# Performance work log

Hardware: AMD Instinct MI355X
Metric: run time of the kernel (lower is better)

The kernel has to match this reference:

```python
import jax, jax.numpy as jnp
import numpy as np

B, C, D, W, H = 8, 256, 24, 24, 24
COUT = 256
EMBED = 128
HEADS = 8
WORD = 64
POOL = 3  # forward hardcodes adaptive_avg_pool3d(x, 3)


def setup_inputs() -> dict:
    key = jax.random.key(0)
    ks = jax.random.split(key, 12)
    s = lambda n: 1.0 / np.sqrt(n)
    return {
        "x": jax.random.normal(ks[0], (B, C, D, W, H), dtype=jnp.float32),
        "qk_w": jax.random.normal(ks[1], (2 * EMBED, POOL ** 3), dtype=jnp.float32) * s(POOL ** 3),
        "qk_b": jax.random.normal(ks[2], (2 * EMBED,), dtype=jnp.float32) * 0.02,
        "wq_w": jax.random.normal(ks[3], (HEADS * WORD, EMBED), dtype=jnp.float32) * s(EMBED),
        "wq_b": jax.random.normal(ks[4], (HEADS * WORD,), dtype=jnp.float32) * 0.02,
        "wk_w": jax.random.normal(ks[5], (HEADS * WORD, EMBED), dtype=jnp.float32) * s(EMBED),
        "wk_b": jax.random.normal(ks[6], (HEADS * WORD,), dtype=jnp.float32) * 0.02,
        "fch_w": jax.random.normal(ks[7], (1, HEADS), dtype=jnp.float32) * s(HEADS),
        "fch_b": jax.random.normal(ks[8], (1,), dtype=jnp.float32) * 0.02,
        "conv_w": jax.random.normal(ks[9], (COUT, C), dtype=jnp.float32) * s(C),
        "conv_b": jax.random.normal(ks[10], (COUT,), dtype=jnp.float32) * 0.02,
    }


def reference(x, qk_w, qk_b, wq_w, wq_b, wk_w, wk_b, fch_w, fch_b, conv_w, conv_b):
    b, c, d, w, h = x.shape
    # adaptive_avg_pool3d to 3x3x3 (exact: dims divisible by 3) -> [b, c, 27]
    xmean = x.reshape(b, c, POOL, d // POOL, POOL, w // POOL, POOL, h // POOL)
    xmean = xmean.mean(axis=(3, 5, 7)).reshape(b, c, POOL ** 3)
    # qk projection -> split into q, k of [b, c, embed]
    qk = xmean @ qk_w.T + qk_b                      # [b, c, 2*embed]
    qk = qk.reshape(b, c, 2, EMBED)
    q, k = qk[:, :, 0], qk[:, :, 1]
    # head projections -> [b, heads, c, word]
    q = (q @ wq_w.T + wq_b).reshape(b, c, HEADS, WORD).transpose(0, 2, 1, 3)
    k = (k @ wk_w.T + wk_b).reshape(b, c, HEADS, WORD).transpose(0, 2, 1, 3)
    # channel attention: scores over channels [b, heads, c, c]
    scores = jnp.einsum("bhcw,bhkw->bhck", q / jnp.sqrt(jnp.float32(WORD)), k)
    attn = jax.nn.softmax(scores, axis=-1)          # dropout is identity in eval
    # v is the raw spatial map [b, c, d*w*h]; broadcast over heads
    v = x.reshape(b, c, d * w * h)
    y = jnp.einsum("bhck,bkn->bhcn", attn, v)       # [b, heads, c, dwh]
    # fch: Linear(heads, 1) combining heads
    y = jnp.einsum("bhcn,h->bcn", y, fch_w[0]) + fch_b[0]
    y = y.reshape(b, c, d, w, h)
    attn_out = jnp.einsum("bhck,h->bck", attn, fch_w[0]) + fch_b[0]  # [b, c, c]
    # 1x1x1 conv residual
    out = jnp.einsum("bcxyz,oc->boxyz", y + x, conv_w) + conv_b[None, :, None, None, None]
    return (out, attn_out)
```

## Files before the change

### kernel.cpp

```cpp
#include <hip/hip_runtime.h>
#include <cstdint>
#include <cstddef>

#define B_    8
#define C_    256
#define DWH   13824
#define P3    27
#define COUT_ 256

#define OFF_XMEAN 0
#define OFF_WQT   55296
#define OFF_WKT   69120
#define OFF_BQ    82944
#define OFF_BK    83456
#define OFF_BETA  83968
#define OFF_G     84224
#define OFF_U     90272
#define OFF_V     90488
#define OFF_D     90704
#define OFF_ZT    90712
#define OFF_A     549464
#define OFF_MPH   1073752
#define OFF_MPL   1335896

typedef __attribute__((ext_vector_type(8))) short bf16x8;
typedef __attribute__((ext_vector_type(4))) float f32x4;

__device__ __forceinline__ void split_bf16(float v, unsigned short& h, unsigned short& l) {
    unsigned u  = __float_as_uint(v);
    unsigned hu = u & 0xFFFF0000u;
    float r = v - __uint_as_float(hu);
    h = (unsigned short)(u >> 16);
    l = (unsigned short)(__float_as_uint(r) >> 16);
}

__device__ __forceinline__ unsigned rne2(float a, float b) {
    unsigned ua = __float_as_uint(a), ub = __float_as_uint(b);
    unsigned ra = (ua + 0x7FFFu + ((ua >> 16) & 1u)) >> 16;
    unsigned rb = (ub + 0x7FFFu + ((ub >> 16) & 1u)) >> 16;
    return ra | (rb << 16);
}

__global__ __launch_bounds__(256) void k_pool(const float* __restrict__ x,
                                              float* __restrict__ xmean) {
    int bc = blockIdx.x;
    __shared__ float p0[576], p1[576], p2[576];
    __shared__ float part[216];
    const float* xb = x + (size_t)bc * DWH;
    for (int t = threadIdx.x; t < 576; t += 256) {
        int g  = t >> 6;
        int s  = t & 63;
        int pd = g / 3, pw = g % 3;
        int d  = pd * 8 + (s >> 3);
        int w  = pw * 8 + (s & 7);
        const float4* r = (const float4*)(xb + ((size_t)d * 24 + w) * 24);
        float4 f0 = r[0], f1 = r[1], f2 = r[2], f3 = r[3], f4v = r[4], f5 = r[5];
        p0[t] = f0.x + f0.y + f0.z + f0.w + f1.x + f1.y + f1.z + f1.w;
        p1[t] = f2.x + f2.y + f2.z + f2.w + f3.x + f3.y + f3.z + f3.w;
        p2[t] = f4v.x + f4v.y + f4v.z + f4v.w + f5.x + f5.y + f5.z + f5.w;
    }
    __syncthreads();
    int tid = threadIdx.x;
    if (tid < 216) {
        int cell = tid >> 3, seg = tid & 7;
        int pd = cell / 9, pw = (cell / 3) % 3, ph = cell % 3;
        int g = pd * 3 + pw;
        const float* src = (ph == 0) ? p0 : (ph == 1 ? p1 : p2);
        float s = 0.f;
        #pragma unroll
        for (int i = 0; i < 8; ++i) s += src[g * 64 + seg * 8 + i];
        part[tid] = s;
    }
    __syncthreads();
    if (tid < 27) {
        float s = 0.f;
        #pragma unroll
        for (int i = 0; i < 8; ++i) s += part[tid * 8 + i];
        xmean[(size_t)bc * P3 + tid] = s * (1.0f / 512.0f);
    }
}

__global__ __launch_bounds__(128) void k_combine(
    const float* __restrict__ qk_w, const float* __restrict__ qk_b,
    const float* __restrict__ wq_w, const float* __restrict__ wq_b,
    const float* __restrict__ wk_w, const float* __restrict__ wk_b,
    float* __restrict__ WqT, float* __restrict__ WkT,
    float* __restrict__ bq, float* __restrict__ bk) {
    int t = blockIdx.x * 128 + threadIdx.x;
    if (t < 13824) {
        int j = t / 27, p = t % 27;
        float s = 0.f;
        for (int e = 0; e < 128; ++e) s += wq_w[j * 128 + e] * qk_w[e * 27 + p];
        WqT[p * 512 + j] = s;
    } else if (t < 27648) {
        int u = t - 13824, j = u / 27, p = u % 27;
        float s = 0.f;
        for (int e = 0; e < 128; ++e) s += wk_w[j * 128 + e] * qk_w[(128 + e) * 27 + p];
        WkT[p * 512 + j] = s;
    } else if (t < 28160) {
        int j = t - 27648;
        float s = wq_b[j];
        for (int e = 0; e < 128; ++e) s += wq_w[j * 128 + e] * qk_b[e];
        bq[j] = s;
    } else if (t < 28672) {
        int j = t - 28160;
        float s = wk_b[j];
        for (int e = 0; e < 128; ++e) s += wk_w[j * 128 + e] * qk_b[128 + e];
        bk[j] = s;
    }
}

__global__ __launch_bounds__(256) void k_G(
    const float* __restrict__ WqT, const float* __restrict__ WkT,
    const float* __restrict__ bq, const float* __restrict__ bk,
    float* __restrict__ G, float* __restrict__ U,
    float* __restrict__ V, float* __restrict__ D) {
    int h = blockIdx.x;
    int idx = blockIdx.y * 256 + threadIdx.x;
    int base = h * 64;
    if (idx < 756) {
        int p = idx / 28, r = idx % 28;
        float s = 0.f;
        if (r < 27) {
            #pragma unroll 8
            for (int w = 0; w < 64; ++w)
                s += WqT[p * 512 + base + w] * WkT[r * 512 + base + w];
        }
        G[(h * 27 + p) * 28 + r] = 0.125f * s;
    } else if (idx < 783) {
        int p = idx - 756;
        float s = 0.f;
        #pragma unroll 8
        for (int w = 0; w < 64; ++w) s += WqT[p * 512 + base + w] * bk[base + w];
        V[h * 27 + p] = 0.125f * s;
    } else if (idx < 810) {
        int r = idx - 783;
        float s = 0.f;
        #pragma unroll 8
        for (int w = 0; w < 64; ++w) s += WkT[r * 512 + base + w] * bq[base + w];
        U[h * 27 + r] = 0.125f * s;
    } else if (idx == 810) {
        float s = 0.f;
        #pragma unroll 8
        for (int w = 0; w < 64; ++w) s += bq[base + w] * bk[base + w];
        D[h] = 0.125f * s;
    }
}

__global__ __launch_bounds__(256) void k_z(
    const float* __restrict__ xmean, const float* __restrict__ G,
    const float* __restrict__ U, const float* __restrict__ V,
    const float* __restrict__ D, float* __restrict__ ZT) {
    int h = blockIdx.x, b = blockIdx.y;
    int k = threadIdx.x;
    __shared__ float Gs[756], Us[27], Vs[27], Ds;
    for (int idx = threadIdx.x; idx < 756; idx += 256) Gs[idx] = G[h * 756 + idx];
    if (threadIdx.x < 27) { Us[threadIdx.x] = U[h * 27 + threadIdx.x];
                            Vs[threadIdx.x] = V[h * 27 + threadIdx.x]; }
    if (threadIdx.x == 27) Ds = D[h];
    __syncthreads();
    float xm[28];
    const float* xp = xmean + ((size_t)(b * C_) + k) * P3;
    #pragma unroll
    for (int r = 0; r < 27; ++r) xm[r] = xp[r];
    xm[27] = 0.f;
    float z[28];
    #pragma unroll
    for (int p = 0; p < 27; ++p) {
        float acc = Vs[p];
        #pragma unroll
        for (int r4 = 0; r4 < 7; ++r4) {
            float4 g = *(const float4*)&Gs[p * 28 + r4 * 4];
            acc += g.x * xm[r4 * 4] + g.y * xm[r4 * 4 + 1]
                 + g.z * xm[r4 * 4 + 2] + g.w * xm[r4 * 4 + 3];
        }
        z[p] = acc;
    }
    {
        float e = Ds;
        #pragma unroll
        for (int r = 0; r < 27; ++r) e += Us[r] * xm[r];
        z[27] = e;
    }
    float4* zt = (float4*)ZT;
    int bh = b * 8 + h;
    #pragma unroll
    for (int p4 = 0; p4 < 7; ++p4) {
        float4 v = {z[p4 * 4], z[p4 * 4 + 1], z[p4 * 4 + 2], z[p4 * 4 + 3]};
        zt[((size_t)(bh * 7 + p4)) * 256 + k] = v;
    }
}

__global__ __launch_bounds__(256) void k_attn(
    const float* __restrict__ xmean, const float* __restrict__ ZT,
    const float* __restrict__ fch_w, const float* __restrict__ fch_b,
    float* __restrict__ A, float* __restrict__ attn_out) {
    int b = blockIdx.y;
    int c0 = blockIdx.x * 4;
    int t = threadIdx.x;
    int lane = t & 63, wv = t >> 6;
    __shared__ float xsh[4 * 28];
    __shared__ float ss[4][256];
    __shared__ float mx[4], den[4];
    if (t < 112) {
        int i = t / 28, p = t % 28;
        xsh[t] = (p < 27) ? xmean[((size_t)(b * C_) + c0 + i) * P3 + p] : 1.0f;
    }
    __syncthreads();
    float4 xr[4][7];
    #pragma unroll
    for (int cl = 0; cl < 4; ++cl)
        #pragma unroll
        for (int p4 = 0; p4 < 7; ++p4)
            xr[cl][p4] = *(const float4*)&xsh[cl * 28 + p4 * 4];
    float areg[4] = {0.f, 0.f, 0.f, 0.f};
    const float4* zt = (const float4*)ZT;
    for (int h = 0; h < 8; ++h) {
        int bh = b * 8 + h;
        float4 zk[7];
        #pragma unroll
        for (int p4 = 0; p4 < 7; ++p4)
            zk[p4] = zt[((size_t)(bh * 7 + p4)) * 256 + t];
        #pragma unroll
        for (int cl = 0; cl < 4; ++cl) {
            float dot = 0.f;
            #pragma unroll
            for (int p4 = 0; p4 < 7; ++p4) {
                float4 xv = xr[cl][p4];
                float4 zv = zk[p4];
                dot += xv.x * zv.x + xv.y * zv.y + xv.z * zv.z + xv.w * zv.w;
            }
            ss[cl][t] = dot;
        }
        __syncthreads();
        {
            int cl = wv;
            float4 v = *(const float4*)&ss[cl][lane * 4];
            float m = fmaxf(fmaxf(v.x, v.y), fmaxf(v.z, v.w));
            for (int off = 32; off; off >>= 1) m = fmaxf(m, __shfl_xor(m, off, 64));
            float s = expf(v.x - m) + expf(v.y - m) + expf(v.z - m) + expf(v.w - m);
            for (int off = 32; off; off >>= 1) s += __shfl_xor(s, off, 64);
            if (lane == 0) { mx[cl] = m; den[cl] = s; }
        }
        __syncthreads();
        float fw = fch_w[h];
        #pragma unroll
        for (int cl = 0; cl < 4; ++cl)
            areg[cl] += expf(ss[cl][t] - mx[cl]) * (fw / den[cl]);
        __syncthreads();
    }
    float fb = fch_b[0];
    #pragma unroll
    for (int cl = 0; cl < 4; ++cl) {
        size_t idx = ((size_t)(b * C_) + c0 + cl) * C_ + t;
        A[idx] = areg[cl];
        attn_out[idx] = areg[cl] + fb;
    }
}

__global__ __launch_bounds__(256) void k_M(
    const float* __restrict__ A, const float* __restrict__ conv_w,
    const float* __restrict__ fch_b, const float* __restrict__ conv_b,
    unsigned short* __restrict__ MpH, unsigned short* __restrict__ MpL,
    float* __restrict__ beta) {
    int b = blockIdx.y;
    int o0 = blockIdx.x * 8;
    int t = threadIdx.x;
    __shared__ float cw[8][256];
    #pragma unroll
    for (int r = 0; r < 8; ++r) cw[r][t] = conv_w[(o0 + r) * 256 + t];
    __syncthreads();
    float acc[8] = {0.f, 0.f, 0.f, 0.f, 0.f, 0.f, 0.f, 0.f};
    const float* Ab = A + (size_t)b * C_ * C_;
    for (int c = 0; c < 256; ++c) {
        float av = Ab[(size_t)c * 256 + t];
        #pragma unroll
        for (int r = 0; r < 8; ++r) acc[r] += cw[r][c] * av;
    }
    if (b == 0 && t < 8) {
        float s = 0.f;
        for (int c = 0; c < 256; ++c) s += cw[t][c];
        beta[o0 + t] = fch_b[0] * s + conv_b[o0 + t];
    }
    int ks = t >> 5, e = t & 7;
    int lanehi = ((t >> 3) & 3) << 4;
    size_t base = ((size_t)(b * 8 + ks) * 16 + (o0 >> 4)) * 64;
    int osub = (o0 & 8);
    #pragma unroll
    for (int r = 0; r < 8; ++r) {
        float mv = acc[r] + cw[r][t];
        unsigned short h, l;
        split_bf16(mv, h, l);
        size_t idx = (base + ((osub + r) | lanehi)) * 8 + e;
        MpH[idx] = h;
        MpL[idx] = l;
    }
}

__global__ __launch_bounds__(256, 3) void k_out_mfma(
    const bf16x8* __restrict__ MpH, const bf16x8* __restrict__ MpL,
    const float* __restrict__ x, const float* __restrict__ beta,
    float* __restrict__ out) {
    int b  = blockIdx.y;
    int n0 = blockIdx.x * 64;
    int t  = threadIdx.x;
    int lane = t & 63, wv = t >> 6;
    int l15  = lane & 15;
    int kseg = lane >> 4;

    __shared__ __align__(16) unsigned short Xs[2][64 * 32];

    f32x4 acc[4][4];
    #pragma unroll
    for (int m = 0; m < 4; ++m)
        #pragma unroll
        for (int nf = 0; nf < 4; ++nf) acc[m][nf] = (f32x4){0.f, 0.f, 0.f, 0.f};

    const float* xb = x + (size_t)b * 256 * DWH;
    const bf16x8* mh = MpH + (size_t)b * 8192;
    const bf16x8* ml = MpL + (size_t)b * 8192;

    int sn = t & 63;
    int sk = t >> 6;
    const float* xcol0 = xb + (size_t)(sk * 8) * DWH + n0 + sn;
    int soff = sn * 64 + ((sk * 16) ^ (((sn >> 1) & 3) << 4));

    {
        float xr[8];
        #pragma unroll
        for (int j = 0; j < 8; ++j) xr[j] = xcol0[(size_t)j * DWH];
        uint4 v;
        v.x = rne2(xr[0], xr[1]); v.y = rne2(xr[2], xr[3]);
        v.z = rne2(xr[4], xr[5]); v.w = rne2(xr[6], xr[7]);
        *(uint4*)((char*)Xs[0] + soff) = v;
    }
    __syncthreads();

    for (int s = 0; s < 8; ++s) {
        int cur = s & 1;
        float xn[8];
        if (s < 7) {
            const float* xc = xcol0 + (size_t)((s + 1) * 32) * DWH;
            #pragma unroll
            for (int j = 0; j < 8; ++j) xn[j] = xc[(size_t)j * DWH];
        }
        bf16x8 Ah[4], Al[4];
        #pragma unroll
        for (int m = 0; m < 4; ++m) {
            int idx = (s * 16 + wv * 4 + m) * 64 + lane;
            Ah[m] = mh[idx];
            Al[m] = ml[idx];
        }
        bf16x8 Bf[4];
        #pragma unroll
        for (int nf = 0; nf < 4; ++nf) {
            int n = nf * 16 + l15;
            int off = n * 64 + ((kseg * 16) ^ (((n >> 1) & 3) << 4));
            Bf[nf] = *(const bf16x8*)((const char*)Xs[cur] + off);
        }
        #pragma unroll
        for (int m = 0; m < 4; ++m)
            #pragma unroll
            for (int nf = 0; nf < 4; ++nf) {
                f32x4 c = acc[m][nf];
                c = __builtin_amdgcn_mfma_f32_16x16x32_bf16(Bf[nf], Al[m], c, 0, 0, 0);
                c = __builtin_amdgcn_mfma_f32_16x16x32_bf16(Bf[nf], Ah[m], c, 0, 0, 0);
                acc[m][nf] = c;
            }
        if (s < 7) {
            uint4 v;
            v.x = rne2(xn[0], xn[1]); v.y = rne2(xn[2], xn[3]);
            v.z = rne2(xn[4], xn[5]); v.w = rne2(xn[6], xn[7]);
            *(uint4*)((char*)Xs[cur ^ 1] + soff) = v;
        }
        __syncthreads();
    }

    int r4 = (lane >> 4) * 4;
    int wo = wv * 64;
    #pragma unroll
    for (int m = 0; m < 4; ++m) {
        int o = wo + m * 16 + l15;
        float bet = beta[o];
        float* orow = out + ((size_t)(b * 256 + o)) * DWH + n0 + r4;
        #pragma unroll
        for (int nf = 0; nf < 4; ++nf) {
            f32x4 c = acc[m][nf];
            float4 v = {c[0] + bet, c[1] + bet, c[2] + bet, c[3] + bet};
            *(float4*)(orow + nf * 16) = v;
        }
    }
}

extern "C" void kernel_launch(void* const* d_in, const int* in_sizes, int n_in,
                              void* d_out, int out_size, void* d_ws, size_t ws_size,
                              hipStream_t stream) {
    const float* x      = (const float*)d_in[0];
    const float* qk_w   = (const float*)d_in[1];
    const float* qk_b   = (const float*)d_in[2];
    const float* wq_w   = (const float*)d_in[3];
    const float* wq_b   = (const float*)d_in[4];
    const float* wk_w   = (const float*)d_in[5];
    const float* wk_b   = (const float*)d_in[6];
    const float* fch_w  = (const float*)d_in[7];
    const float* fch_b  = (const float*)d_in[8];
    const float* conv_w = (const float*)d_in[9];
    const float* conv_b = (const float*)d_in[10];
    float* out = (float*)d_out;
    float* attn_out = out + (size_t)B_ * COUT_ * DWH;
    float* ws = (float*)d_ws;
    unsigned short* MpH = (unsigned short*)(ws + OFF_MPH);
    unsigned short* MpL = (unsigned short*)(ws + OFF_MPL);

    k_pool<<<B_ * C_, 256, 0, stream>>>(x, ws + OFF_XMEAN);
    k_combine<<<224, 128, 0, stream>>>(qk_w, qk_b, wq_w, wq_b, wk_w, wk_b,
                                       ws + OFF_WQT, ws + OFF_WKT,
                                       ws + OFF_BQ, ws + OFF_BK);
    k_G<<<dim3(8, 4), 256, 0, stream>>>(ws + OFF_WQT, ws + OFF_WKT,
                                        ws + OFF_BQ, ws + OFF_BK,
                                        ws + OFF_G, ws + OFF_U, ws + OFF_V, ws + OFF_D);
    k_z<<<dim3(8, B_), 256, 0, stream>>>(ws + OFF_XMEAN, ws + OFF_G, ws + OFF_U,
                                         ws + OFF_V, ws + OFF_D, ws + OFF_ZT);
    k_attn<<<dim3(64, B_), 256, 0, stream>>>(ws + OFF_XMEAN, ws + OFF_ZT, fch_w, fch_b,
                                             ws + OFF_A, attn_out);
    k_M<<<dim3(32, B_), 256, 0, stream>>>(ws + OFF_A, conv_w, fch_b, conv_b,
                                          MpH, MpL, ws + OFF_BETA);
    k_out_mfma<<<dim3(216, B_), 256, 0, stream>>>((const bf16x8*)MpH, (const bf16x8*)MpL,
                                                  x, ws + OFF_BETA, out);
}
```

Measured before the change: 126.2 us.

## Fuse pooling and weight-combine kernels; batch softmax across heads in attention

```diff
diff --git a/kernel.cpp b/kernel.cpp
--- a/kernel.cpp
+++ b/kernel.cpp
@@ -41,72 +41,73 @@
     return ra | (rb << 16);
 }
 
-__global__ __launch_bounds__(256) void k_pool(const float* __restrict__ x,
-                                              float* __restrict__ xmean) {
-    int bc = blockIdx.x;
-    __shared__ float p0[576], p1[576], p2[576];
-    __shared__ float part[216];
-    const float* xb = x + (size_t)bc * DWH;
-    for (int t = threadIdx.x; t < 576; t += 256) {
-        int g  = t >> 6;
-        int s  = t & 63;
-        int pd = g / 3, pw = g % 3;
-        int d  = pd * 8 + (s >> 3);
-        int w  = pw * 8 + (s & 7);
-        const float4* r = (const float4*)(xb + ((size_t)d * 24 + w) * 24);
-        float4 f0 = r[0], f1 = r[1], f2 = r[2], f3 = r[3], f4v = r[4], f5 = r[5];
-        p0[t] = f0.x + f0.y + f0.z + f0.w + f1.x + f1.y + f1.z + f1.w;
-        p1[t] = f2.x + f2.y + f2.z + f2.w + f3.x + f3.y + f3.z + f3.w;
-        p2[t] = f4v.x + f4v.y + f4v.z + f4v.w + f5.x + f5.y + f5.z + f5.w;
-    }
-    __syncthreads();
-    int tid = threadIdx.x;
-    if (tid < 216) {
-        int cell = tid >> 3, seg = tid & 7;
-        int pd = cell / 9, pw = (cell / 3) % 3, ph = cell % 3;
-        int g = pd * 3 + pw;
-        const float* src = (ph == 0) ? p0 : (ph == 1 ? p1 : p2);
-        float s = 0.f;
-        #pragma unroll
-        for (int i = 0; i < 8; ++i) s += src[g * 64 + seg * 8 + i];
-        part[tid] = s;
-    }
-    __syncthreads();
-    if (tid < 27) {
-        float s = 0.f;
-        #pragma unroll
-        for (int i = 0; i < 8; ++i) s += part[tid * 8 + i];
-        xmean[(size_t)bc * P3 + tid] = s * (1.0f / 512.0f);
-    }
-}
-
-__global__ __launch_bounds__(128) void k_combine(
+__global__ __launch_bounds__(256) void k_front(
+    const float* __restrict__ x,
     const float* __restrict__ qk_w, const float* __restrict__ qk_b,
     const float* __restrict__ wq_w, const float* __restrict__ wq_b,
     const float* __restrict__ wk_w, const float* __restrict__ wk_b,
+    float* __restrict__ xmean,
     float* __restrict__ WqT, float* __restrict__ WkT,
     float* __restrict__ bq, float* __restrict__ bk) {
-    int t = blockIdx.x * 128 + threadIdx.x;
-    if (t < 13824) {
-        int j = t / 27, p = t % 27;
-        float s = 0.f;
-        for (int e = 0; e < 128; ++e) s += wq_w[j * 128 + e] * qk_w[e * 27 + p];
-        WqT[p * 512 + j] = s;
-    } else if (t < 27648) {
-        int u = t - 13824, j = u / 27, p = u % 27;
-        float s = 0.f;
-        for (int e = 0; e < 128; ++e) s += wk_w[j * 128 + e] * qk_w[(128 + e) * 27 + p];
-        WkT[p * 512 + j] = s;
-    } else if (t < 28160) {
-        int j = t - 27648;
-        float s = wq_b[j];
-        for (int e = 0; e < 128; ++e) s += wq_w[j * 128 + e] * qk_b[e];
-        bq[j] = s;
-    } else if (t < 28672) {
-        int j = t - 28160;
-        float s = wk_b[j];
-        for (int e = 0; e < 128; ++e) s += wk_w[j * 128 + e] * qk_b[128 + e];
-        bk[j] = s;
+    __shared__ float p0[576], p1[576], p2[576];
+    __shared__ float part[216];
+    if (blockIdx.x < 2048) {
+        int bc = blockIdx.x;
+        const float* xb = x + (size_t)bc * DWH;
+        for (int t = threadIdx.x; t < 576; t += 256) {
+            int g  = t >> 6;
+            int s  = t & 63;
+            int pd = g / 3, pw = g % 3;
+            int d  = pd * 8 + (s >> 3);
+            int w  = pw * 8 + (s & 7);
+            const float4* r = (const float4*)(xb + ((size_t)d * 24 + w) * 24);
+            float4 f0 = r[0], f1 = r[1], f2 = r[2], f3 = r[3], f4v = r[4], f5 = r[5];
+            p0[t] = f0.x + f0.y + f0.z + f0.w + f1.x + f1.y + f1.z + f1.w;
+            p1[t] = f2.x + f2.y + f2.z + f2.w + f3.x + f3.y + f3.z + f3.w;
+            p2[t] = f4v.x + f4v.y + f4v.z + f4v.w + f5.x + f5.y + f5.z + f5.w;
+        }
+        __syncthreads();
+        int tid = threadIdx.x;
+        if (tid < 216) {
+            int cell = tid >> 3, seg = tid & 7;
+            int pd = cell / 9, pw = (cell / 3) % 3, ph = cell % 3;
+            int g = pd * 3 + pw;
+            const float* src = (ph == 0) ? p0 : (ph == 1 ? p1 : p2);
+            float s = 0.f;
+            #pragma unroll
+            for (int i = 0; i < 8; ++i) s += src[g * 64 + seg * 8 + i];
+            part[tid] = s;
+        }
+        __syncthreads();
+        if (tid < 27) {
+            float s = 0.f;
+            #pragma unroll
+            for (int i = 0; i < 8; ++i) s += part[tid * 8 + i];
+            xmean[(size_t)bc * P3 + tid] = s * (1.0f / 512.0f);
+        }
+    } else {
+        int t = (blockIdx.x - 2048) * 256 + threadIdx.x;
+        if (t < 13824) {
+            int j = t / 27, p = t % 27;
+            float s = 0.f;
+            for (int e = 0; e < 128; ++e) s += wq_w[j * 128 + e] * qk_w[e * 27 + p];
+            WqT[p * 512 + j] = s;
+        } else if (t < 27648) {
+            int u = t - 13824, j = u / 27, p = u % 27;
+            float s = 0.f;
+            for (int e = 0; e < 128; ++e) s += wk_w[j * 128 + e] * qk_w[(128 + e) * 27 + p];
+            WkT[p * 512 + j] = s;
+        } else if (t < 28160) {
+            int j = t - 27648;
+            float s = wq_b[j];
+            for (int e = 0; e < 128; ++e) s += wq_w[j * 128 + e] * qk_b[e];
+            bq[j] = s;
+        } else if (t < 28672) {
+            int j = t - 28160;
+            float s = wk_b[j];
+            for (int e = 0; e < 128; ++e) s += wk_w[j * 128 + e] * qk_b[128 + e];
+            bk[j] = s;
+        }
     }
 }
 
@@ -200,20 +201,13 @@
     int t = threadIdx.x;
     int lane = t & 63, wv = t >> 6;
     __shared__ float xsh[4 * 28];
-    __shared__ float ss[4][256];
-    __shared__ float mx[4], den[4];
+    __shared__ float ss[8][4][256];
+    __shared__ float mx[8][4], scl[8][4];
     if (t < 112) {
         int i = t / 28, p = t % 28;
         xsh[t] = (p < 27) ? xmean[((size_t)(b * C_) + c0 + i) * P3 + p] : 1.0f;
     }
     __syncthreads();
-    float4 xr[4][7];
-    #pragma unroll
-    for (int cl = 0; cl < 4; ++cl)
-        #pragma unroll
-        for (int p4 = 0; p4 < 7; ++p4)
-            xr[cl][p4] = *(const float4*)&xsh[cl * 28 + p4 * 4];
-    float areg[4] = {0.f, 0.f, 0.f, 0.f};
     const float4* zt = (const float4*)ZT;
     for (int h = 0; h < 8; ++h) {
         int bh = b * 8 + h;
@@ -226,29 +220,32 @@
             float dot = 0.f;
             #pragma unroll
             for (int p4 = 0; p4 < 7; ++p4) {
-                float4 xv = xr[cl][p4];
+                float4 xv = *(const float4*)&xsh[cl * 28 + p4 * 4];
                 float4 zv = zk[p4];
                 dot += xv.x * zv.x + xv.y * zv.y + xv.z * zv.z + xv.w * zv.w;
             }
-            ss[cl][t] = dot;
-        }
-        __syncthreads();
-        {
-            int cl = wv;
-            float4 v = *(const float4*)&ss[cl][lane * 4];
-            float m = fmaxf(fmaxf(v.x, v.y), fmaxf(v.z, v.w));
-            for (int off = 32; off; off >>= 1) m = fmaxf(m, __shfl_xor(m, off, 64));
-            float s = expf(v.x - m) + expf(v.y - m) + expf(v.z - m) + expf(v.w - m);
-            for (int off = 32; off; off >>= 1) s += __shfl_xor(s, off, 64);
-            if (lane == 0) { mx[cl] = m; den[cl] = s; }
-        }
-        __syncthreads();
-        float fw = fch_w[h];
+            ss[h][cl][t] = dot;
+        }
+    }
+    __syncthreads();
+    #pragma unroll
+    for (int j = 0; j < 8; ++j) {
+        int pr = wv * 8 + j;
+        int h = pr >> 2, cl = pr & 3;
+        float4 v = *(const float4*)&ss[h][cl][lane * 4];
+        float m = fmaxf(fmaxf(v.x, v.y), fmaxf(v.z, v.w));
+        for (int off = 32; off; off >>= 1) m = fmaxf(m, __shfl_xor(m, off, 64));
+        float s = expf(v.x - m) + expf(v.y - m) + expf(v.z - m) + expf(v.w - m);
+        for (int off = 32; off; off >>= 1) s += __shfl_xor(s, off, 64);
+        if (lane == 0) { mx[h][cl] = m; scl[h][cl] = fch_w[h] / s; }
+    }
+    __syncthreads();
+    float areg[4] = {0.f, 0.f, 0.f, 0.f};
+    #pragma unroll
+    for (int h = 0; h < 8; ++h)
         #pragma unroll
         for (int cl = 0; cl < 4; ++cl)
-            areg[cl] += expf(ss[cl][t] - mx[cl]) * (fw / den[cl]);
-        __syncthreads();
-    }
+            areg[cl] += expf(ss[h][cl][t] - mx[h][cl]) * scl[h][cl];
     float fb = fch_b[0];
     #pragma unroll
     for (int cl = 0; cl < 4; ++cl) {
@@ -412,10 +409,9 @@
     unsigned short* MpH = (unsigned short*)(ws + OFF_MPH);
     unsigned short* MpL = (unsigned short*)(ws + OFF_MPL);
 
-    k_pool<<<B_ * C_, 256, 0, stream>>>(x, ws + OFF_XMEAN);
-    k_combine<<<224, 128, 0, stream>>>(qk_w, qk_b, wq_w, wq_b, wk_w, wk_b,
-                                       ws + OFF_WQT, ws + OFF_WKT,
-                                       ws + OFF_BQ, ws + OFF_BK);
+    k_front<<<2160, 256, 0, stream>>>(x, qk_w, qk_b, wq_w, wq_b, wk_w, wk_b,
+                                      ws + OFF_XMEAN, ws + OFF_WQT, ws + OFF_WKT,
+                                      ws + OFF_BQ, ws + OFF_BK);
     k_G<<<dim3(8, 4), 256, 0, stream>>>(ws + OFF_WQT, ws + OFF_WKT,
                                         ws + OFF_BQ, ws + OFF_BK,
                                         ws + OFF_G, ws + OFF_U, ws + OFF_V, ws + OFF_D);
```

After: 141.5 us. 1.12x slower.
